# Optimization experiments

Hardware: AMD Instinct MI355X
Metric: run time of the kernel (lower is better)

Reference implementation:

```python
import jax, jax.numpy as jnp
import numpy as np

LATENT_DIM = 128
NUM_QUANTIZERS = 8
CODEBOOK_SIZE = 1024


def setup_inputs() -> dict:
    key = jax.random.key(0)
    k1, k2 = jax.random.split(key)
    z = jax.random.normal(k1, (8, LATENT_DIM, 4096), dtype=jnp.float32)
    scale = 1.0 / np.sqrt(LATENT_DIM)
    codebooks = jax.random.uniform(
        k2, (NUM_QUANTIZERS, CODEBOOK_SIZE, LATENT_DIM),
        minval=-scale, maxval=scale, dtype=jnp.float32)
    return {"z": z, "codebooks": codebooks}


def _nearest_indices(x_flat, codebook):
    # x_flat: [N, D], codebook: [K, D] -> [N] argmin of squared L2 distance
    d = (jnp.sum(x_flat * x_flat, axis=1, keepdims=True)
         - 2.0 * x_flat @ codebook.T
         + jnp.sum(codebook * codebook, axis=1)[None, :])
    return jnp.argmin(d, axis=1)


def reference(z, codebooks):
    # z: [B, D, S] -> z_bsd: [B, S, D]
    z_bsd = jnp.transpose(z, (0, 2, 1))
    B, S, D = z_bsd.shape
    Q, K, _ = codebooks.shape

    residual = z_bsd
    quantized = jnp.zeros_like(z_bsd)
    idx_list = []
    for q in range(Q):  # small fixed loop over quantizer stages
        cb = codebooks[q]
        idx = _nearest_indices(residual.reshape(-1, D), cb).reshape(B, S)
        selected = cb[idx]                       # [B, S, D] gather
        quantized = quantized + selected
        residual = residual - jax.lax.stop_gradient(selected)
        idx_list.append(idx)
    indices = jnp.stack(idx_list, axis=-1)        # [B, S, Q]

    commitment_loss = jnp.mean(
        (z_bsd - jax.lax.stop_gradient(quantized)) ** 2)
    quantized_st = z_bsd + jax.lax.stop_gradient(quantized - z_bsd)

    def _perplexity(ix):  # ix: [B, S] codes for one quantizer
        counts = jnp.zeros((K,), jnp.float32).at[ix.reshape(-1)].add(1.0)
        probs = counts / jnp.maximum(counts.sum(), 1.0)
        entropy = -jnp.sum(probs * jnp.log(probs + 1e-10))
        return jnp.exp(entropy)

    perplexity = jnp.mean(jax.vmap(_perplexity, in_axes=2)(indices))

    return (jnp.transpose(quantized_st, (0, 2, 1)),  # [B, D, S]
            indices, commitment_loss, perplexity)
```

## Files before the change

### kernel.cpp

```cpp
#include <hip/hip_runtime.h>
#include <math.h>
#include <stdint.h>

#define D       128
#define KCODES  1024
#define NQ      8
#define BATCH   8
#define SLEN    4096
#define NPTS    (BATCH*SLEN)
#define TM      64

typedef __attribute__((address_space(1))) const void GV;
typedef __attribute__((address_space(3))) void LV;
__device__ __forceinline__ void gload16(const void* g, void* l) {
    __builtin_amdgcn_global_load_lds((GV*)g, (LV*)l, 16, 0, 0);
}

__global__ void k_zero(int* hist, double* csum) {
    int t = blockIdx.x * blockDim.x + threadIdx.x;
    if (t < NQ * KCODES) hist[t] = 0;
    if (t == 0) *csum = 0.0;
}

__global__ void k_c2(const float* __restrict__ cbs, float* __restrict__ c2f) {
    int i = blockIdx.x * blockDim.x + threadIdx.x;
    const float* row = cbs + (size_t)i * D;
    float r8[8];
    #pragma unroll
    for (int j = 0; j < 8; ++j) r8[j] = __fmul_rn(row[j], row[j]);
    for (int d = 8; d < 128; d += 8)
        #pragma unroll
        for (int j = 0; j < 8; ++j)
            r8[j] = __fadd_rn(r8[j], __fmul_rn(row[d + j], row[d + j]));
    float s01 = __fadd_rn(r8[0], r8[1]);
    float s23 = __fadd_rn(r8[2], r8[3]);
    float s45 = __fadd_rn(r8[4], r8[5]);
    float s67 = __fadd_rn(r8[6], r8[7]);
    c2f[i] = __fadd_rn(__fadd_rn(s01, s23), __fadd_rn(s45, s67));
}

__global__ __launch_bounds__(256) void k_init(const float* __restrict__ z,
                                              float* __restrict__ resid,
                                              float* __restrict__ quant) {
    __shared__ float xt[64][129];
    int b = blockIdx.x >> 6, st = blockIdx.x & 63;
    int s0 = st * 64;
    for (int it = 0; it < 32; ++it) {
        int flat = it * 256 + threadIdx.x;
        int d = flat >> 6, sl = flat & 63;
        xt[sl][d] = z[((size_t)(b * D + d)) * SLEN + s0 + sl];
    }
    __syncthreads();
    for (int it = 0; it < 8; ++it) {
        int flat = it * 256 + threadIdx.x;
        int sl = flat >> 5, dq = (flat & 31) * 4;
        size_t o = (size_t)(b * SLEN + s0 + sl) * D + dq;
        float4 r;
        r.x = xt[sl][dq]; r.y = xt[sl][dq + 1];
        r.z = xt[sl][dq + 2]; r.w = xt[sl][dq + 3];
        *(float4*)(resid + o) = r;
        float4 zz; zz.x = zz.y = zz.z = zz.w = 0.0f;
        *(float4*)(quant + o) = zz;
    }
}

__global__ __launch_bounds__(256) void k_argmin(const float* __restrict__ cb,
                                                const float* __restrict__ c2,
                                                const float* __restrict__ resid,
                                                float* __restrict__ pbest,
                                                int* __restrict__ pidx) {
    __shared__ __align__(16) float xs[TM][132];
    __shared__ __align__(16) float cs[4][2][512];
    __shared__ __align__(16) float ccl[4][128];
    __shared__ float redS[4][TM];
    __shared__ int   redI[4][TM];

    int tid = threadIdx.x;
    int u = blockIdx.x;
    int pblk = u >> 1, half = u & 1;
    int pbase = pblk * TM;
    int l = tid & 63, w = tid >> 6;
    int pl = l & 7, cl = l >> 3;

    const char* cwb = (const char*)cb + ((size_t)(half * 512 + w * 128) << 9);
    char* csw = (char*)&cs[w][0][0];
    const char* xsb = (const char*)&xs[0][0];

#define ISSUE(S) { \
    const char* _src = cwb + ((size_t)l << 9) + ((S) << 4); \
    char* _dst = csw + (((S) & 1) << 11); \
    gload16(_src,             _dst); \
    gload16(_src + (1 << 15), _dst + 1024); }

    ISSUE(0);
    if (l < 32) {
        float4 cv = *(const float4*)(c2 + half * 512 + w * 128 + l * 4);
        *(float4*)&ccl[w][l * 4] = cv;
    }

    #pragma unroll
    for (int it = 0; it < 8; ++it) {
        int e = (it * 256 + tid) * 4;
        int p = e >> 7, d = e & 127;
        *(float4*)&xs[p][d] = *(const float4*)(resid + (size_t)(pbase + p) * D + d);
    }
    __syncthreads();

    if (tid < TM) {
        float r8[8];
        #pragma unroll
        for (int j = 0; j < 8; ++j) r8[j] = __fmul_rn(xs[tid][j], xs[tid][j]);
        for (int i = 8; i < 128; i += 8)
            #pragma unroll
            for (int j = 0; j < 8; ++j)
                r8[j] = __fadd_rn(r8[j], __fmul_rn(xs[tid][i + j], xs[tid][i + j]));
        float s01 = __fadd_rn(r8[0], r8[1]);
        float s23 = __fadd_rn(r8[2], r8[3]);
        float s45 = __fadd_rn(r8[4], r8[5]);
        float s67 = __fadd_rn(r8[6], r8[7]);
        xs[tid][128] = __fadd_rn(__fadd_rn(s01, s23), __fadd_rn(s45, s67));
    }
    __syncthreads();

    float xxr[8];
    #pragma unroll
    for (int i = 0; i < 8; ++i) xxr[i] = xs[pl + 8 * i][128];

    float acc[8][16];
    #pragma unroll
    for (int i = 0; i < 8; ++i)
        #pragma unroll
        for (int j = 0; j < 16; ++j) acc[i][j] = 0.0f;
    float best[8]; int bidx[8];
    #pragma unroll
    for (int i = 0; i < 8; ++i) { best[i] = 3.4e38f; bidx[i] = 0; }

    #pragma unroll 1
    for (int t = 0; t < 32; ++t) {
        if (t < 31) {
            ISSUE(t + 1);
            asm volatile("s_waitcnt vmcnt(2)" ::: "memory");
        } else {
            asm volatile("s_waitcnt vmcnt(0)" ::: "memory");
        }
        const char* cbuf = csw + ((t & 1) << 11) + (cl << 4);
        const char* xrow = xsb + pl * 528 + (t << 4);
        float4 xf[8];
        #pragma unroll
        for (int i = 0; i < 8; ++i)
            xf[i] = *(const float4*)(xrow + i * 4224);
        #pragma unroll
        for (int jb = 0; jb < 4; ++jb) {
            float4 cf[4];
            #pragma unroll
            for (int j = 0; j < 4; ++j)
                cf[j] = *(const float4*)(cbuf + ((jb * 4 + j) << 7));
            #pragma unroll
            for (int j = 0; j < 4; ++j) {
                int jj = jb * 4 + j;
                #pragma unroll
                for (int i = 0; i < 8; ++i) {
                    acc[i][jj] = __fmaf_rn(xf[i].x, cf[j].x, acc[i][jj]);
                    acc[i][jj] = __fmaf_rn(xf[i].y, cf[j].y, acc[i][jj]);
                    acc[i][jj] = __fmaf_rn(xf[i].z, cf[j].z, acc[i][jj]);
                    acc[i][jj] = __fmaf_rn(xf[i].w, cf[j].w, acc[i][jj]);
                }
            }
        }
    }

    #pragma unroll
    for (int j = 0; j < 16; ++j) {
        float cc = ccl[w][cl + (j << 3)];
        int k = half * 512 + (w << 7) + cl + (j << 3);
        #pragma unroll
        for (int i = 0; i < 8; ++i) {
            float t1  = __fadd_rn(xxr[i], __fmul_rn(-2.0f, acc[i][j]));
            float dsc = __fadd_rn(t1, cc);
            if (dsc < best[i]) { best[i] = dsc; bidx[i] = k; }
        }
    }

    #pragma unroll
    for (int i = 0; i < 8; ++i) {
        float b = best[i]; int bi = bidx[i];
        #pragma unroll
        for (int off = 8; off < 64; off <<= 1) {
            float b2 = __shfl_xor(b, off, 64);
            int  bi2 = __shfl_xor(bi, off, 64);
            if (b2 < b || (b2 == b && bi2 < bi)) { b = b2; bi = bi2; }
        }
        if (cl == 0) { redS[w][pl + 8 * i] = b; redI[w][pl + 8 * i] = bi; }
    }
    __syncthreads();
    if (tid < TM) {
        float b = redS[0][tid]; int bi = redI[0][tid];
        #pragma unroll
        for (int ww = 1; ww < 4; ++ww) {
            float b2 = redS[ww][tid]; int bi2 = redI[ww][tid];
            if (b2 < b || (b2 == b && bi2 < bi)) { b = b2; bi = bi2; }
        }
        pbest[half * NPTS + pbase + tid] = b;
        pidx [half * NPTS + pbase + tid] = bi;
    }
#undef ISSUE
}

__global__ void k_merge(const float* __restrict__ pbest, const int* __restrict__ pidx,
                        int* __restrict__ idxq) {
    int n = blockIdx.x * blockDim.x + threadIdx.x;
    float a = pbest[n], b = pbest[NPTS + n];
    int ia = pidx[n], ib = pidx[NPTS + n];
    idxq[n] = (b < a) ? ib : ia;
}

__global__ void k_update(const float* __restrict__ cb, const int* __restrict__ idx,
                         float* __restrict__ resid, float* __restrict__ quant) {
    int gid = blockIdx.x * blockDim.x + threadIdx.x;
    int n = gid >> 5, d4 = (gid & 31) * 4;
    int k = idx[n];
    float4 c = *(const float4*)(cb + (size_t)k * D + d4);
    size_t o = (size_t)n * D + d4;
    float4 r = *(const float4*)(resid + o);
    float4 q = *(const float4*)(quant + o);
    r.x = __fsub_rn(r.x, c.x); r.y = __fsub_rn(r.y, c.y);
    r.z = __fsub_rn(r.z, c.z); r.w = __fsub_rn(r.w, c.w);
    q.x = __fadd_rn(q.x, c.x); q.y = __fadd_rn(q.y, c.y);
    q.z = __fadd_rn(q.z, c.z); q.w = __fadd_rn(q.w, c.w);
    *(float4*)(resid + o) = r;
    *(float4*)(quant + o) = q;
}

__global__ __launch_bounds__(256) void k_out0(const float* __restrict__ z,
                                              const float* __restrict__ quant,
                                              float* __restrict__ out0,
                                              double* __restrict__ csum) {
    __shared__ float xt[64][129];
    __shared__ double wsum[4];
    int b = blockIdx.x >> 6, st = blockIdx.x & 63;
    int s0 = st * 64;
    for (int it = 0; it < 8; ++it) {
        int flat = it * 256 + threadIdx.x;
        int sl = flat >> 5, dq = (flat & 31) * 4;
        float4 q = *(const float4*)(quant + (size_t)(b * SLEN + s0 + sl) * D + dq);
        xt[sl][dq] = q.x; xt[sl][dq + 1] = q.y;
        xt[sl][dq + 2] = q.z; xt[sl][dq + 3] = q.w;
    }
    __syncthreads();
    double v = 0.0;
    for (int it = 0; it < 32; ++it) {
        int flat = it * 256 + threadIdx.x;
        int d = flat >> 6, sl = flat & 63;
        size_t o = ((size_t)(b * D + d)) * SLEN + s0 + sl;
        float zz = z[o], qq = xt[sl][d];
        out0[o] = __fadd_rn(zz, __fsub_rn(qq, zz));
        float e = __fsub_rn(zz, qq);
        v += (double)e * (double)e;
    }
    for (int off = 32; off > 0; off >>= 1) v += __shfl_down(v, off, 64);
    int lane = threadIdx.x & 63, wv = threadIdx.x >> 6;
    if (lane == 0) wsum[wv] = v;
    __syncthreads();
    if (threadIdx.x == 0) {
        double tsum = wsum[0] + wsum[1] + wsum[2] + wsum[3];
        atomicAdd(csum, tsum);
    }
}

__global__ void k_outidx(const int* __restrict__ idx, float* __restrict__ out1) {
    int o = blockIdx.x * blockDim.x + threadIdx.x;
    int q = o & 7, n = o >> 3;
    out1[o] = (float)idx[q * NPTS + n];
}

__global__ void k_hist(const int* __restrict__ idx, int* __restrict__ hist) {
    int o = blockIdx.x * blockDim.x + threadIdx.x;
    int q = o >> 15;
    atomicAdd(&hist[q * KCODES + idx[o]], 1);
}

__global__ __launch_bounds__(256) void k_final(const int* __restrict__ hist,
                                               const double* __restrict__ csum,
                                               float* __restrict__ outs) {
    __shared__ double sh[256];
    double perp = 0.0;
    for (int q = 0; q < NQ; ++q) {
        double h = 0.0;
        for (int k = threadIdx.x; k < KCODES; k += 256) {
            double p = (double)hist[q * KCODES + k] / (double)NPTS;
            h -= p * log(p + 1e-10);
        }
        sh[threadIdx.x] = h; __syncthreads();
        for (int off = 128; off > 0; off >>= 1) {
            if (threadIdx.x < off) sh[threadIdx.x] += sh[threadIdx.x + off];
            __syncthreads();
        }
        if (threadIdx.x == 0) perp += exp(sh[0]);
        __syncthreads();
    }
    if (threadIdx.x == 0) {
        outs[0] = (float)(*csum / (double)((size_t)NPTS * D));
        outs[1] = (float)(perp / (double)NQ);
    }
}

extern "C" void kernel_launch(void* const* d_in, const int* in_sizes, int n_in,
                              void* d_out, int out_size, void* d_ws, size_t ws_size,
                              hipStream_t stream) {
    const float* z  = (const float*)d_in[0];
    const float* cb = (const float*)d_in[1];
    float* out0 = (float*)d_out;
    float* out1 = out0 + 4194304;
    float* outs = out1 + 262144;

    char* w = (char*)d_ws;
    float* resid  = (float*)w;
    float* quant  = (float*)(w + 16777216);
    int*   idx    = (int*)(w + 33554432);
    int*   hist   = (int*)(w + 34603008);
    double* csum  = (double*)(w + 34635776);
    float* c2f    = (float*)(w + 34635840);
    float* pbest  = (float*)(w + 34668608);
    int*   pidx   = (int*)(w + 34930752);

    k_zero<<<32, 256, 0, stream>>>(hist, csum);
    k_c2<<<32, 256, 0, stream>>>(cb, c2f);
    k_init<<<512, 256, 0, stream>>>(z, resid, quant);

    for (int q = 0; q < NQ; ++q) {
        const float* cbq = cb + (size_t)q * KCODES * D;
        k_argmin<<<2 * NPTS / TM, 256, 0, stream>>>(cbq, c2f + q * KCODES, resid,
                                                    pbest, pidx);
        k_merge<<<NPTS / 256, 256, 0, stream>>>(pbest, pidx, idx + q * NPTS);
        k_update<<<NPTS * 32 / 256, 256, 0, stream>>>(cbq, idx + q * NPTS,
                                                      resid, quant);
    }

    k_out0<<<512, 256, 0, stream>>>(z, quant, out0, csum);
    k_outidx<<<NPTS * NQ / 256, 256, 0, stream>>>(idx, out1);
    k_hist<<<NPTS * NQ / 256, 256, 0, stream>>>(idx, hist);
    k_final<<<1, 256, 0, stream>>>(hist, csum, outs);
}
```

Measured before the change: 1.168 ms.

## Halve argmin accumulator tile for two-wave occupancy and fuse merge into update

The argmin kernel now holds 8x8 accumulators instead of 8x16 and walks each wave's 128 codes in two 64-code chunks, reducing to best/index after each chunk. Its codebook double buffer shrinks to 1 KB per wave with one async load per step, and the launch bounds request two blocks per SIMD, all to cut register and LDS pressure and raise occupancy. The separate merge kernel is removed: k_update now picks between the two half results itself and writes the index, saving one launch and one pass over memory per stage. The cost is twice as many loop steps with more load/wait overhead, and x values are re-read from LDS for each chunk.

```diff
diff --git a/kernel.cpp b/kernel.cpp
--- a/kernel.cpp
+++ b/kernel.cpp
@@ -64,13 +64,13 @@
     }
 }
 
-__global__ __launch_bounds__(256) void k_argmin(const float* __restrict__ cb,
-                                                const float* __restrict__ c2,
-                                                const float* __restrict__ resid,
-                                                float* __restrict__ pbest,
-                                                int* __restrict__ pidx) {
+__global__ __launch_bounds__(256, 2) void k_argmin(const float* __restrict__ cb,
+                                                   const float* __restrict__ c2,
+                                                   const float* __restrict__ resid,
+                                                   float* __restrict__ pbest,
+                                                   int* __restrict__ pidx) {
     __shared__ __align__(16) float xs[TM][132];
-    __shared__ __align__(16) float cs[4][2][512];
+    __shared__ __align__(16) float cs[4][2][256];
     __shared__ __align__(16) float ccl[4][128];
     __shared__ float redS[4][TM];
     __shared__ int   redI[4][TM];
@@ -86,11 +86,9 @@
     char* csw = (char*)&cs[w][0][0];
     const char* xsb = (const char*)&xs[0][0];
 
-#define ISSUE(S) { \
-    const char* _src = cwb + ((size_t)l << 9) + ((S) << 4); \
-    char* _dst = csw + (((S) & 1) << 11); \
-    gload16(_src,             _dst); \
-    gload16(_src + (1 << 15), _dst + 1024); }
+#define ISSUE(T) { \
+    const char* _src = cwb + (((T) >> 5) << 15) + ((size_t)l << 9) + (((T) & 31) << 4); \
+    gload16(_src, csw + (((T) & 1) << 10)); }
 
     ISSUE(0);
     if (l < 32) {
@@ -126,58 +124,59 @@
     #pragma unroll
     for (int i = 0; i < 8; ++i) xxr[i] = xs[pl + 8 * i][128];
 
-    float acc[8][16];
+    float acc[8][8];
     #pragma unroll
     for (int i = 0; i < 8; ++i)
         #pragma unroll
-        for (int j = 0; j < 16; ++j) acc[i][j] = 0.0f;
+        for (int j = 0; j < 8; ++j) acc[i][j] = 0.0f;
     float best[8]; int bidx[8];
     #pragma unroll
     for (int i = 0; i < 8; ++i) { best[i] = 3.4e38f; bidx[i] = 0; }
 
     #pragma unroll 1
-    for (int t = 0; t < 32; ++t) {
-        if (t < 31) {
+    for (int t = 0; t < 64; ++t) {
+        if (t < 63) {
             ISSUE(t + 1);
-            asm volatile("s_waitcnt vmcnt(2)" ::: "memory");
+            asm volatile("s_waitcnt vmcnt(1)" ::: "memory");
         } else {
             asm volatile("s_waitcnt vmcnt(0)" ::: "memory");
         }
-        const char* cbuf = csw + ((t & 1) << 11) + (cl << 4);
-        const char* xrow = xsb + pl * 528 + (t << 4);
+        const char* cbuf = csw + ((t & 1) << 10) + (cl << 4);
+        const char* xrow = xsb + pl * 528 + ((t & 31) << 4);
         float4 xf[8];
         #pragma unroll
         for (int i = 0; i < 8; ++i)
             xf[i] = *(const float4*)(xrow + i * 4224);
         #pragma unroll
-        for (int jb = 0; jb < 4; ++jb) {
-            float4 cf[4];
+        for (int jp = 0; jp < 4; ++jp) {
+            float4 cf0 = *(const float4*)(cbuf + ((2 * jp)     << 7));
+            float4 cf1 = *(const float4*)(cbuf + ((2 * jp + 1) << 7));
             #pragma unroll
-            for (int j = 0; j < 4; ++j)
-                cf[j] = *(const float4*)(cbuf + ((jb * 4 + j) << 7));
+            for (int i = 0; i < 8; ++i) {
+                acc[i][2*jp]   = __fmaf_rn(xf[i].x, cf0.x, acc[i][2*jp]);
+                acc[i][2*jp]   = __fmaf_rn(xf[i].y, cf0.y, acc[i][2*jp]);
+                acc[i][2*jp]   = __fmaf_rn(xf[i].z, cf0.z, acc[i][2*jp]);
+                acc[i][2*jp]   = __fmaf_rn(xf[i].w, cf0.w, acc[i][2*jp]);
+                acc[i][2*jp+1] = __fmaf_rn(xf[i].x, cf1.x, acc[i][2*jp+1]);
+                acc[i][2*jp+1] = __fmaf_rn(xf[i].y, cf1.y, acc[i][2*jp+1]);
+                acc[i][2*jp+1] = __fmaf_rn(xf[i].z, cf1.z, acc[i][2*jp+1]);
+                acc[i][2*jp+1] = __fmaf_rn(xf[i].w, cf1.w, acc[i][2*jp+1]);
+            }
+        }
+        if ((t & 31) == 31) {
+            int c = t >> 5;
             #pragma unroll
-            for (int j = 0; j < 4; ++j) {
-                int jj = jb * 4 + j;
+            for (int j = 0; j < 8; ++j) {
+                float cc = ccl[w][(c << 6) + cl + (j << 3)];
+                int k = half * 512 + (w << 7) + (c << 6) + cl + (j << 3);
                 #pragma unroll
                 for (int i = 0; i < 8; ++i) {
-                    acc[i][jj] = __fmaf_rn(xf[i].x, cf[j].x, acc[i][jj]);
-                    acc[i][jj] = __fmaf_rn(xf[i].y, cf[j].y, acc[i][jj]);
-                    acc[i][jj] = __fmaf_rn(xf[i].z, cf[j].z, acc[i][jj]);
-                    acc[i][jj] = __fmaf_rn(xf[i].w, cf[j].w, acc[i][jj]);
+                    float t1  = __fadd_rn(xxr[i], __fmul_rn(-2.0f, acc[i][j]));
+                    float dsc = __fadd_rn(t1, cc);
+                    if (dsc < best[i]) { best[i] = dsc; bidx[i] = k; }
+                    acc[i][j] = 0.0f;
                 }
             }
-        }
-    }
-
-    #pragma unroll
-    for (int j = 0; j < 16; ++j) {
-        float cc = ccl[w][cl + (j << 3)];
-        int k = half * 512 + (w << 7) + cl + (j << 3);
-        #pragma unroll
-        for (int i = 0; i < 8; ++i) {
-            float t1  = __fadd_rn(xxr[i], __fmul_rn(-2.0f, acc[i][j]));
-            float dsc = __fadd_rn(t1, cc);
-            if (dsc < best[i]) { best[i] = dsc; bidx[i] = k; }
         }
     }
 
@@ -206,19 +205,17 @@
 #undef ISSUE
 }
 
-__global__ void k_merge(const float* __restrict__ pbest, const int* __restrict__ pidx,
-                        int* __restrict__ idxq) {
-    int n = blockIdx.x * blockDim.x + threadIdx.x;
-    float a = pbest[n], b = pbest[NPTS + n];
-    int ia = pidx[n], ib = pidx[NPTS + n];
-    idxq[n] = (b < a) ? ib : ia;
-}
-
-__global__ void k_update(const float* __restrict__ cb, const int* __restrict__ idx,
+__global__ void k_update(const float* __restrict__ cb,
+                         const float* __restrict__ pbest,
+                         const int* __restrict__ pidx,
+                         int* __restrict__ idx,
                          float* __restrict__ resid, float* __restrict__ quant) {
     int gid = blockIdx.x * blockDim.x + threadIdx.x;
     int n = gid >> 5, d4 = (gid & 31) * 4;
-    int k = idx[n];
+    float a = pbest[n], b = pbest[NPTS + n];
+    int ia = pidx[n], ib = pidx[NPTS + n];
+    int k = (b < a) ? ib : ia;
+    if ((gid & 31) == 0) idx[n] = k;
     float4 c = *(const float4*)(cb + (size_t)k * D + d4);
     size_t o = (size_t)n * D + d4;
     float4 r = *(const float4*)(resid + o);
@@ -331,9 +328,8 @@
         const float* cbq = cb + (size_t)q * KCODES * D;
         k_argmin<<<2 * NPTS / TM, 256, 0, stream>>>(cbq, c2f + q * KCODES, resid,
                                                     pbest, pidx);
-        k_merge<<<NPTS / 256, 256, 0, stream>>>(pbest, pidx, idx + q * NPTS);
-        k_update<<<NPTS * 32 / 256, 256, 0, stream>>>(cbq, idx + q * NPTS,
-                                                      resid, quant);
+        k_update<<<NPTS * 32 / 256, 256, 0, stream>>>(cbq, pbest, pidx,
+                                                      idx + q * NPTS, resid, quant);
     }
 
     k_out0<<<512, 256, 0, stream>>>(z, quant, out0, csum);
```

After: 1.167 ms. Within noise of the previous version (-0.2%).
